# Kernel tuning notes

Measured on AMD Instinct MI355X. Metric: run time of the kernel, lower is better.

Reference implementation:

```python
import jax, jax.numpy as jnp
import numpy as np

DIM = 1024
N_STATE = 64
T, B = 512, 32


def _xavier(key, shape):
    fan_out, fan_in = shape
    limit = np.sqrt(6.0 / (fan_in + fan_out)).astype(np.float32)
    return jax.random.uniform(key, shape, jnp.float32, -limit, limit)


def setup_inputs() -> dict:
    key = jax.random.key(0)
    ks = jax.random.split(key, 5)
    return {
        "x": jax.random.normal(ks[0], (T, B, DIM), jnp.float32),
        "S": jnp.zeros((B, N_STATE, N_STATE), jnp.float32),
        "W_k": _xavier(ks[1], (N_STATE, DIM)),
        "W_v": _xavier(ks[2], (N_STATE, DIM)),
        "W_q": _xavier(ks[3], (N_STATE, DIM)),
        "W_alpha": _xavier(ks[4], (N_STATE, DIM)),
        "d_alpha": jnp.full((N_STATE,), 0.1, jnp.float32),
        "b_alpha": jnp.full((N_STATE,), 2.0, jnp.float32),
    }


def reference(x, S, W_k, W_v, W_q, W_alpha, d_alpha, b_alpha):
    # Precompute all projections as batched GEMMs: [T,B,n_state]
    k = jnp.einsum("tbd,nd->tbn", x, W_k)
    v = jnp.einsum("tbd,nd->tbn", x, W_v)
    q = jnp.einsum("tbd,nd->tbn", x, W_q)
    ax = jnp.einsum("tbd,nd->tbn", x, W_alpha)

    def step(S, inp):
        k_t, v_t, q_t, ax_t = inp  # each [B, n_state]
        retrieved = jnp.einsum("bij,bj->bi", S, k_t)          # S @ k
        alpha = jax.nn.sigmoid(ax_t + d_alpha * retrieved + b_alpha)
        # S = alpha * S + (1 - alpha) * outer(v, k); alpha gates rows
        S_new = alpha[:, :, None] * S + (1.0 - alpha)[:, :, None] * (
            v_t[:, :, None] * k_t[:, None, :]
        )
        h = jnp.einsum("bij,bj->bi", S_new, q_t)              # S @ q
        out_t = h * jax.nn.silu(h)                             # self-gated output
        return S_new, out_t

    S_final, output = jax.lax.scan(step, S, (k, v, q, ax))
    return output, S_final
```

## Files before the change

### kernel.cpp

```cpp
#include <hip/hip_runtime.h>
#include <hip/hip_bf16.h>

#define T_STEPS 512
#define BATCH 32
#define NST 64
#define DIM 1024

typedef _Float16 f16x8 __attribute__((ext_vector_type(8)));
typedef _Float16 f16x4 __attribute__((ext_vector_type(4)));
typedef float f32x4 __attribute__((ext_vector_type(4)));
typedef float f32x2 __attribute__((ext_vector_type(2)));

__device__ __forceinline__ void gl_lds16(const void* g, void* l) {
  __builtin_amdgcn_global_load_lds(
      (const __attribute__((address_space(1))) void*)g,
      (__attribute__((address_space(3))) void*)l, 16, 0, 0);
}

__global__ __launch_bounds__(256) void wconv(
    const float* __restrict__ Wk, const float* __restrict__ Wv,
    const float* __restrict__ Wq, const float* __restrict__ Wa,
    _Float16* __restrict__ Wc) {
  const int n = blockIdx.x;
  const int g = n >> 6, r = n & 63;
  const float* W = (g == 0) ? Wk : (g == 1) ? Wq : (g == 2) ? Wv : Wa;
  const float sc = (g == 3) ? -1.44269504088896340736f : 1.0f;
  float4 v = *(const float4*)(W + (size_t)r * DIM + threadIdx.x * 4);
  f16x4 h = {(_Float16)(v.x * sc), (_Float16)(v.y * sc), (_Float16)(v.z * sc),
             (_Float16)(v.w * sc)};
  *(f16x4*)(Wc + (size_t)n * DIM + threadIdx.x * 4) = h;
}

__global__ __launch_bounds__(512) void proj_gemm(
    const float* __restrict__ x, const _Float16* __restrict__ Wc,
    float* __restrict__ projf) {
  const int m0 = blockIdx.x * 64;
  const int tid = threadIdx.x;
  const int lane = tid & 63, wv = tid >> 6;
  const int wm = wv >> 2, wn = wv & 3;
  const int fm = lane & 15, fq = lane >> 4;

  __shared__ __align__(16) _Float16 Bl[2][256 * 32];
  __shared__ __align__(16) _Float16 Al[2][64 * 32];

  const int brow = tid >> 2;
  const int bcg = (tid & 3) ^ ((tid >> 3) & 3);
  const _Float16* gB = Wc + (size_t)brow * DIM + bcg * 8;
  const int bdst = tid * 8;

#define STAGE_B(buf, k0)                                          \
  {                                                               \
    _Pragma("unroll") for (int i = 0; i < 2; ++i)                 \
        gl_lds16(gB + (size_t)i * 128 * DIM + (k0),               \
                 &Bl[buf][i * 4096 + bdst]);                      \
  }

  const int arow = tid >> 3;
  const int afc = (tid & 7) * 4;
  const float* gA = x + (size_t)(m0 + arow) * DIM + afc;
  const int awp = arow * 32 + ((((tid >> 1) & 3) ^ ((arow >> 1) & 3)) * 8) +
                  (tid & 1) * 4;

#define LOADX(rr, k0)                          \
  {                                            \
    rr = *(const float4*)(gA + (k0));          \
  }
#define CVT_WRITE_A(buf, rr)                                        \
  {                                                                 \
    f16x4 h = {(_Float16)rr.x, (_Float16)rr.y, (_Float16)rr.z,      \
               (_Float16)rr.w};                                     \
    *(f16x4*)&Al[buf][awp] = h;                                     \
  }

  f32x4 acc[2][4];
#pragma unroll
  for (int mi = 0; mi < 2; ++mi)
#pragma unroll
    for (int ni = 0; ni < 4; ++ni) acc[mi][ni] = (f32x4){0.f, 0.f, 0.f, 0.f};

  const int aswz = (fq ^ ((fm >> 1) & 3)) * 8;
  const int abase = (wm * 32 + fm) * 32 + aswz;
  const int bbase = (wn * 64 + fm) * 32 + aswz;

#define COMPUTE(cb)                                                     \
  {                                                                     \
    f16x8 afr[2], bfr[4];                                               \
    _Pragma("unroll") for (int mi = 0; mi < 2; ++mi)                    \
        afr[mi] = *(const f16x8*)&Al[cb][abase + mi * 16 * 32];         \
    _Pragma("unroll") for (int ni = 0; ni < 4; ++ni)                    \
        bfr[ni] = *(const f16x8*)&Bl[cb][bbase + ni * 16 * 32];         \
    _Pragma("unroll") for (int mi = 0; mi < 2; ++mi)                    \
        _Pragma("unroll") for (int ni = 0; ni < 4; ++ni)                \
            acc[mi][ni] = __builtin_amdgcn_mfma_f32_16x16x32_f16(       \
                afr[mi], bfr[ni], acc[mi][ni], 0, 0, 0);                \
  }

  float4 rE, rO;
  LOADX(rE, 0);
  STAGE_B(0, 0);
  LOADX(rO, 32);
  CVT_WRITE_A(0, rE);
  __syncthreads();

  for (int k2 = 0; k2 < 16; ++k2) {
    STAGE_B(1, (2 * k2 + 1) * 32);
    if (k2 < 15) LOADX(rE, (2 * k2 + 2) * 32);
    CVT_WRITE_A(1, rO);
    COMPUTE(0);
    __syncthreads();
    if (k2 < 15) {
      STAGE_B(0, (2 * k2 + 2) * 32);
      LOADX(rO, (2 * k2 + 3) * 32);
      CVT_WRITE_A(0, rE);
    }
    COMPUTE(1);
    __syncthreads();
  }
#undef STAGE_B
#undef LOADX
#undef CVT_WRITE_A
#undef COMPUTE

#pragma unroll
  for (int mi = 0; mi < 2; ++mi)
#pragma unroll
    for (int ni = 0; ni < 4; ++ni) {
      const int gcol = wn * 64 + ni * 16 + fm;
      const int pcol = gcol < 128 ? gcol
                     : (gcol < 192 ? 128 + 2 * (gcol - 128) : 129 + 2 * (gcol - 192));
#pragma unroll
      for (int r = 0; r < 4; ++r) {
        const int grow = m0 + wm * 32 + mi * 16 + fq * 4 + r;
        projf[(size_t)grow * 256 + pcol] = acc[mi][ni][r];
      }
    }
}

__device__ __forceinline__ float red16(float x) {
  int v = __builtin_amdgcn_update_dpp(0, __float_as_int(x), 0xB1, 0xF, 0xF, true);
  x += __int_as_float(v);
  v = __builtin_amdgcn_update_dpp(0, __float_as_int(x), 0x4E, 0xF, 0xF, true);
  x += __int_as_float(v);
  v = __builtin_amdgcn_update_dpp(0, __float_as_int(x), 0x124, 0xF, 0xF, true);
  x += __int_as_float(v);
  v = __builtin_amdgcn_update_dpp(0, __float_as_int(x), 0x128, 0xF, 0xF, true);
  x += __int_as_float(v);
  return x;
}

__global__ __launch_bounds__(512, 1) void scan_kernel(
    const float* __restrict__ projf, const float* __restrict__ S0,
    const float* __restrict__ d_alpha, const float* __restrict__ b_alpha,
    float* __restrict__ out, float* __restrict__ Sout) {
  const int b = blockIdx.x >> 2;
  const int rg = blockIdx.x & 3;
  const int tid = threadIdx.x;
  const bool prod = tid < 256;
  const int ptid = tid & 255;
  const int c = ptid & 15;
  const int lr = ptid >> 4;
  const int r = rg * 16 + lr;
  const int j0 = c * 4;

  __shared__ __align__(16) float lbuf[4][2048];
  __shared__ __align__(16) float2 alcc[2][8][16];

  constexpr float NL2E = -1.44269504088896340736f;
  f32x2 s01, s23;
  {
    float4 v = *(const float4*)(S0 + ((size_t)b * NST + r) * NST + j0);
    s01 = (f32x2){v.x, v.y}; s23 = (f32x2){v.z, v.w};
  }
  const float da2 = d_alpha[r] * NL2E;
  const float ba2 = b_alpha[r] * NL2E;

  const int sstep = tid >> 6;
  const int soff = (tid & 63) * 4;
  const int lidx = sstep * 256 + soff;
  const float* gp = projf + (size_t)b * 256;
#define GADDR(ch) (gp + (size_t)((ch) * 8 + sstep) * (BATCH * 256) + soff)

  float4 rA;
  rA = *(const float4*)GADDR(0); *(float4*)&lbuf[0][lidx] = rA;
  rA = *(const float4*)GADDR(1); *(float4*)&lbuf[1][lidx] = rA;
  rA = *(const float4*)GADDR(2);
  __syncthreads();

  f32x2 k01[2], k23[2], q01[2], q23[2], vaf[2];
#define PREFP(tn)                                                        \
  {                                                                      \
    const int pp = (tn) & 1;                                             \
    const float* Pn = &lbuf[((tn) >> 3) & 3][((tn) & 7) * 256];          \
    float4 kk = *(const float4*)(Pn + j0);                               \
    k01[pp] = (f32x2){kk.x, kk.y}; k23[pp] = (f32x2){kk.z, kk.w};        \
    float2 vv = *(const float2*)(Pn + 128 + 2 * r);                      \
    vaf[pp] = (f32x2){vv.x, vv.y};                                       \
  }
#define PREFC(tn)                                                        \
  {                                                                      \
    const int pp = (tn) & 1;                                             \
    const float* Pn = &lbuf[((tn) >> 3) & 3][((tn) & 7) * 256];          \
    float4 kk = *(const float4*)(Pn + j0);                               \
    k01[pp] = (f32x2){kk.x, kk.y}; k23[pp] = (f32x2){kk.z, kk.w};        \
    float4 qq = *(const float4*)(Pn + 64 + j0);                          \
    q01[pp] = (f32x2){qq.x, qq.y}; q23[pp] = (f32x2){qq.z, qq.w};        \
  }

  if (prod) { PREFP(0); } else { PREFC(0); }

  for (int ch = 0; ch <= 64; ++ch) {
    if (prod) {
      if (ch < 64) {
#pragma unroll
        for (int si = 0; si < 8; ++si) {
          const int t = ch * 8 + si;
          const int p = si & 1;
          if (t + 1 < T_STEPS) PREFP(t + 1);

          f32x2 pa = s01 * k01[p] + s23 * k23[p];
          const float rr = red16(pa[0] + pa[1]);

          float z2 = fmaf(da2, rr, vaf[p][1] + ba2);
          z2 = __builtin_amdgcn_fmed3f(z2, -43.3f, 43.3f);
          const float e = __builtin_amdgcn_exp2f(z2);
          const float al = __builtin_amdgcn_rcpf(1.f + e);
          const float cc = (e * vaf[p][0]) * al;

          const f32x2 al2 = {al, al}, cc2 = {cc, cc};
          s01 = al2 * s01 + cc2 * k01[p];
          s23 = al2 * s23 + cc2 * k23[p];

          if (c == 0) alcc[ch & 1][si][lr] = make_float2(al, cc);
        }
      }
    } else {
      if (ch >= 1) {
        const int pch = ch - 1;
#pragma unroll
        for (int si = 0; si < 8; ++si) {
          const int t = pch * 8 + si;
          const int p = si & 1;
          if (t + 1 < T_STEPS) PREFC(t + 1);

          float2 ac = alcc[pch & 1][si][lr];
          const f32x2 al2 = {ac.x, ac.x}, cc2 = {ac.y, ac.y};
          s01 = al2 * s01 + cc2 * k01[p];
          s23 = al2 * s23 + cc2 * k23[p];

          f32x2 hh = s01 * q01[p] + s23 * q23[p];
          const float h = red16(hh[0] + hh[1]);
          if (c == 0) {
            const float sg =
                __builtin_amdgcn_rcpf(1.f + __builtin_amdgcn_exp2f(h * NL2E));
            out[((size_t)t * BATCH + b) * NST + r] = (h * h) * sg;
          }
        }
      }
    }
    __syncthreads();
    if (ch + 2 < 64) *(float4*)&lbuf[(ch + 2) & 3][lidx] = rA;
    if (ch + 3 < 64) rA = *(const float4*)GADDR(ch + 3);
    __syncthreads();
  }
#undef PREFP
#undef PREFC
#undef GADDR

  if (!prod) {
    float4 o = {s01[0], s01[1], s23[0], s23[1]};
    *(float4*)(Sout + ((size_t)b * NST + r) * NST + j0) = o;
  }
}

extern "C" void kernel_launch(void* const* d_in, const int* in_sizes, int n_in,
                              void* d_out, int out_size, void* d_ws, size_t ws_size,
                              hipStream_t stream) {
  const float* x  = (const float*)d_in[0];
  const float* S0 = (const float*)d_in[1];
  const float* Wk = (const float*)d_in[2];
  const float* Wv = (const float*)d_in[3];
  const float* Wq = (const float*)d_in[4];
  const float* Wa = (const float*)d_in[5];
  const float* da = (const float*)d_in[6];
  const float* ba = (const float*)d_in[7];

  float* out  = (float*)d_out;
  float* Sout = out + (size_t)T_STEPS * BATCH * NST;
  float* projf = (float*)d_ws;
  _Float16* Wc = (_Float16*)((char*)d_ws + (size_t)16384 * 256 * 4);

  wconv<<<256, 256, 0, stream>>>(Wk, Wv, Wq, Wa, Wc);
  proj_gemm<<<256, 512, 0, stream>>>(x, Wc, projf);
  scan_kernel<<<4 * BATCH, 512, 0, stream>>>(projf, S0, da, ba, out, Sout);
}
```

Before: 210.6 us.

## Replace LDS staging of projections with direct register double-buffered global loads

The scan kernel stops staging projection chunks through a 32KB shared buffer. Producer and consumer threads now load their own k/v/q slices for 8 timesteps straight from global memory into register arrays, double-buffered across two chunks. The alpha/c handoff buffer is transposed so consumers can read all 8 steps for their row at once. This removes the LDS round trip and some copy work, but raises register pressure and may expose global load latency on the serial scan path.

```diff
diff --git a/kernel.cpp b/kernel.cpp
--- a/kernel.cpp
+++ b/kernel.cpp
@@ -162,8 +162,7 @@
   const int r = rg * 16 + lr;
   const int j0 = c * 4;
 
-  __shared__ __align__(16) float lbuf[4][2048];
-  __shared__ __align__(16) float2 alcc[2][8][16];
+  __shared__ __align__(16) float2 alcc[2][16][8];
 
   constexpr float NL2E = -1.44269504088896340736f;
   f32x2 s01, s23;
@@ -174,102 +173,102 @@
   const float da2 = d_alpha[r] * NL2E;
   const float ba2 = b_alpha[r] * NL2E;
 
-  const int sstep = tid >> 6;
-  const int soff = (tid & 63) * 4;
-  const int lidx = sstep * 256 + soff;
-  const float* gp = projf + (size_t)b * 256;
-#define GADDR(ch) (gp + (size_t)((ch) * 8 + sstep) * (BATCH * 256) + soff)
-
-  float4 rA;
-  rA = *(const float4*)GADDR(0); *(float4*)&lbuf[0][lidx] = rA;
-  rA = *(const float4*)GADDR(1); *(float4*)&lbuf[1][lidx] = rA;
-  rA = *(const float4*)GADDR(2);
-  __syncthreads();
-
-  f32x2 k01[2], k23[2], q01[2], q23[2], vaf[2];
-#define PREFP(tn)                                                        \
-  {                                                                      \
-    const int pp = (tn) & 1;                                             \
-    const float* Pn = &lbuf[((tn) >> 3) & 3][((tn) & 7) * 256];          \
-    float4 kk = *(const float4*)(Pn + j0);                               \
-    k01[pp] = (f32x2){kk.x, kk.y}; k23[pp] = (f32x2){kk.z, kk.w};        \
-    float2 vv = *(const float2*)(Pn + 128 + 2 * r);                      \
-    vaf[pp] = (f32x2){vv.x, vv.y};                                       \
-  }
-#define PREFC(tn)                                                        \
-  {                                                                      \
-    const int pp = (tn) & 1;                                             \
-    const float* Pn = &lbuf[((tn) >> 3) & 3][((tn) & 7) * 256];          \
-    float4 kk = *(const float4*)(Pn + j0);                               \
-    k01[pp] = (f32x2){kk.x, kk.y}; k23[pp] = (f32x2){kk.z, kk.w};        \
-    float4 qq = *(const float4*)(Pn + 64 + j0);                          \
-    q01[pp] = (f32x2){qq.x, qq.y}; q23[pp] = (f32x2){qq.z, qq.w};        \
-  }
-
-  if (prod) { PREFP(0); } else { PREFC(0); }
-
-  for (int ch = 0; ch <= 64; ++ch) {
+  const float* gb = projf + (size_t)b * 256;
+
+#define P_LOAD(karr, varr, chn)                                         \
+  {                                                                     \
+    const float* pb = gb + (size_t)(chn) * 65536;                       \
+    _Pragma("unroll") for (int si = 0; si < 8; ++si) {                  \
+      karr[si] = *(const float4*)(pb + si * 8192 + j0);                 \
+      varr[si] = *(const float2*)(pb + si * 8192 + 128 + 2 * r);        \
+    }                                                                   \
+  }
+#define C_LOAD(karr, qarr, chn)                                         \
+  {                                                                     \
+    const float* pb = gb + (size_t)(chn) * 65536;                       \
+    _Pragma("unroll") for (int si = 0; si < 8; ++si) {                  \
+      karr[si] = *(const float4*)(pb + si * 8192 + j0);                 \
+      qarr[si] = *(const float4*)(pb + si * 8192 + 64 + j0);            \
+    }                                                                   \
+  }
+
+#define P_COMP(karr, varr, abuf)                                        \
+  {                                                                     \
+    _Pragma("unroll") for (int si = 0; si < 8; ++si) {                  \
+      const f32x2 k01 = {karr[si].x, karr[si].y};                       \
+      const f32x2 k23 = {karr[si].z, karr[si].w};                       \
+      f32x2 pa = s01 * k01 + s23 * k23;                                 \
+      const float rr = red16(pa[0] + pa[1]);                            \
+      float z2 = fmaf(da2, rr, varr[si].y + ba2);                       \
+      z2 = __builtin_amdgcn_fmed3f(z2, -43.3f, 43.3f);                  \
+      const float e = __builtin_amdgcn_exp2f(z2);                       \
+      const float al = __builtin_amdgcn_rcpf(1.f + e);                  \
+      const float ccv = (e * varr[si].x) * al;                          \
+      const f32x2 al2 = {al, al}, cc2 = {ccv, ccv};                     \
+      s01 = al2 * s01 + cc2 * k01;                                      \
+      s23 = al2 * s23 + cc2 * k23;                                      \
+      if (c == 0) alcc[abuf][lr][si] = make_float2(al, ccv);            \
+    }                                                                   \
+  }
+#define C_COMP(karr, qarr, abuf, chn)                                   \
+  {                                                                     \
+    float2 acv[8];                                                      \
+    _Pragma("unroll") for (int si = 0; si < 8; ++si)                    \
+        acv[si] = alcc[abuf][lr][si];                                   \
+    _Pragma("unroll") for (int si = 0; si < 8; ++si) {                  \
+      const f32x2 k01 = {karr[si].x, karr[si].y};                       \
+      const f32x2 k23 = {karr[si].z, karr[si].w};                       \
+      const f32x2 al2 = {acv[si].x, acv[si].x};                         \
+      const f32x2 cc2 = {acv[si].y, acv[si].y};                         \
+      s01 = al2 * s01 + cc2 * k01;                                      \
+      s23 = al2 * s23 + cc2 * k23;                                      \
+      const f32x2 q01 = {qarr[si].x, qarr[si].y};                       \
+      const f32x2 q23 = {qarr[si].z, qarr[si].w};                       \
+      f32x2 hh = s01 * q01 + s23 * q23;                                 \
+      const float h = red16(hh[0] + hh[1]);                             \
+      if (c == 0) {                                                     \
+        const float sg =                                                \
+            __builtin_amdgcn_rcpf(1.f + __builtin_amdgcn_exp2f(h * NL2E)); \
+        out[((size_t)((chn) * 8 + si) * BATCH + b) * NST + r] = (h * h) * sg; \
+      }                                                                 \
+    }                                                                   \
+  }
+
+  float4 kA[8], kB[8];
+  float2 vA[8], vB[8];
+  float4 qA[8], qB[8];
+
+  if (prod) {
+    P_LOAD(kA, vA, 0);
+  }
+
+  for (int c2 = 0; c2 < 32; ++c2) {
     if (prod) {
-      if (ch < 64) {
-#pragma unroll
-        for (int si = 0; si < 8; ++si) {
-          const int t = ch * 8 + si;
-          const int p = si & 1;
-          if (t + 1 < T_STEPS) PREFP(t + 1);
-
-          f32x2 pa = s01 * k01[p] + s23 * k23[p];
-          const float rr = red16(pa[0] + pa[1]);
-
-          float z2 = fmaf(da2, rr, vaf[p][1] + ba2);
-          z2 = __builtin_amdgcn_fmed3f(z2, -43.3f, 43.3f);
-          const float e = __builtin_amdgcn_exp2f(z2);
-          const float al = __builtin_amdgcn_rcpf(1.f + e);
-          const float cc = (e * vaf[p][0]) * al;
-
-          const f32x2 al2 = {al, al}, cc2 = {cc, cc};
-          s01 = al2 * s01 + cc2 * k01[p];
-          s23 = al2 * s23 + cc2 * k23[p];
-
-          if (c == 0) alcc[ch & 1][si][lr] = make_float2(al, cc);
-        }
-      }
+      P_LOAD(kB, vB, 2 * c2 + 1);
+      P_COMP(kA, vA, 0);
     } else {
-      if (ch >= 1) {
-        const int pch = ch - 1;
-#pragma unroll
-        for (int si = 0; si < 8; ++si) {
-          const int t = pch * 8 + si;
-          const int p = si & 1;
-          if (t + 1 < T_STEPS) PREFC(t + 1);
-
-          float2 ac = alcc[pch & 1][si][lr];
-          const f32x2 al2 = {ac.x, ac.x}, cc2 = {ac.y, ac.y};
-          s01 = al2 * s01 + cc2 * k01[p];
-          s23 = al2 * s23 + cc2 * k23[p];
-
-          f32x2 hh = s01 * q01[p] + s23 * q23[p];
-          const float h = red16(hh[0] + hh[1]);
-          if (c == 0) {
-            const float sg =
-                __builtin_amdgcn_rcpf(1.f + __builtin_amdgcn_exp2f(h * NL2E));
-            out[((size_t)t * BATCH + b) * NST + r] = (h * h) * sg;
-          }
-        }
-      }
-    }
-    __syncthreads();
-    if (ch + 2 < 64) *(float4*)&lbuf[(ch + 2) & 3][lidx] = rA;
-    if (ch + 3 < 64) rA = *(const float4*)GADDR(ch + 3);
-    __syncthreads();
-  }
-#undef PREFP
-#undef PREFC
-#undef GADDR
-
+      C_LOAD(kA, qA, 2 * c2);
+      if (c2 > 0) C_COMP(kB, qB, 1, 2 * c2 - 1);
+    }
+    __syncthreads();
+    if (prod) {
+      if (c2 < 31) P_LOAD(kA, vA, 2 * c2 + 2);
+      P_COMP(kB, vB, 1);
+    } else {
+      C_LOAD(kB, qB, 2 * c2 + 1);
+      C_COMP(kA, qA, 0, 2 * c2);
+    }
+    __syncthreads();
+  }
   if (!prod) {
+    C_COMP(kB, qB, 1, 63);
     float4 o = {s01[0], s01[1], s23[0], s23[1]};
     *(float4*)(Sout + ((size_t)b * NST + r) * NST + j0) = o;
   }
+#undef P_LOAD
+#undef C_LOAD
+#undef P_COMP
+#undef C_COMP
 }
 
 extern "C" void kernel_launch(void* const* d_in, const int* in_sizes, int n_in,
```

After: 237.7 us. +12.9%, slower.

## Break scan dependency chain using precomputed consecutive-key dot products

Applied to the files above, without the earlier changes.

Adds a small kernel that computes k_{t-1}·k_t for every batch and timestep and stages it in LDS. The producer wavefront then computes the retrieval S_t·k_t algebraically from the previous step's quantities (alpha, e, v and the Gram value) plus a reduction on the already-updated state for the next key. This takes the cross-lane reduction off the critical serial path between consecutive steps. It costs an extra kernel launch, a deeper four-slot prefetch buffer, and a different floating-point summation order in the recurrence.

```diff
diff --git a/kernel.cpp b/kernel.cpp
--- a/kernel.cpp
+++ b/kernel.cpp
@@ -136,6 +136,27 @@
     }
 }
 
+__global__ __launch_bounds__(256) void gram_kernel(
+    const float* __restrict__ projf, float* __restrict__ gmat) {
+  const int b = blockIdx.x >> 1;
+  const int t = (blockIdx.x & 1) * 256 + threadIdx.x;
+  float acc = 0.f;
+  if (t > 0) {
+    const float* ka = projf + ((size_t)(t - 1) * BATCH + b) * 256;
+    const float* kb = projf + ((size_t)t * BATCH + b) * 256;
+#pragma unroll
+    for (int j = 0; j < 64; j += 4) {
+      float4 va = *(const float4*)(ka + j);
+      float4 vb = *(const float4*)(kb + j);
+      acc = fmaf(va.x, vb.x, acc);
+      acc = fmaf(va.y, vb.y, acc);
+      acc = fmaf(va.z, vb.z, acc);
+      acc = fmaf(va.w, vb.w, acc);
+    }
+  }
+  gmat[(size_t)b * T_STEPS + t] = acc;
+}
+
 __device__ __forceinline__ float red16(float x) {
   int v = __builtin_amdgcn_update_dpp(0, __float_as_int(x), 0xB1, 0xF, 0xF, true);
   x += __int_as_float(v);
@@ -149,7 +170,8 @@
 }
 
 __global__ __launch_bounds__(512, 1) void scan_kernel(
-    const float* __restrict__ projf, const float* __restrict__ S0,
+    const float* __restrict__ projf, const float* __restrict__ gmat,
+    const float* __restrict__ S0,
     const float* __restrict__ d_alpha, const float* __restrict__ b_alpha,
     float* __restrict__ out, float* __restrict__ Sout) {
   const int b = blockIdx.x >> 2;
@@ -164,6 +186,7 @@
 
   __shared__ __align__(16) float lbuf[4][2048];
   __shared__ __align__(16) float2 alcc[2][8][16];
+  __shared__ __align__(8) float glds[T_STEPS];
 
   constexpr float NL2E = -1.44269504088896340736f;
   f32x2 s01, s23;
@@ -180,33 +203,48 @@
   const float* gp = projf + (size_t)b * 256;
 #define GADDR(ch) (gp + (size_t)((ch) * 8 + sstep) * (BATCH * 256) + soff)
 
+  glds[tid] = gmat[(size_t)b * T_STEPS + tid];
+
   float4 rA;
   rA = *(const float4*)GADDR(0); *(float4*)&lbuf[0][lidx] = rA;
   rA = *(const float4*)GADDR(1); *(float4*)&lbuf[1][lidx] = rA;
   rA = *(const float4*)GADDR(2);
   __syncthreads();
 
-  f32x2 k01[2], k23[2], q01[2], q23[2], vaf[2];
+  float4 kf[4];
+  float2 vaf[4];
+  float gv[4];
 #define PREFP(tn)                                                        \
   {                                                                      \
-    const int pp = (tn) & 1;                                             \
+    const int pp = (tn) & 3;                                             \
     const float* Pn = &lbuf[((tn) >> 3) & 3][((tn) & 7) * 256];          \
-    float4 kk = *(const float4*)(Pn + j0);                               \
-    k01[pp] = (f32x2){kk.x, kk.y}; k23[pp] = (f32x2){kk.z, kk.w};        \
-    float2 vv = *(const float2*)(Pn + 128 + 2 * r);                      \
-    vaf[pp] = (f32x2){vv.x, vv.y};                                       \
-  }
+    kf[pp] = *(const float4*)(Pn + j0);                                  \
+    vaf[pp] = *(const float2*)(Pn + 128 + 2 * r);                        \
+    gv[pp] = glds[(tn)];                                                 \
+  }
+  float4 kc4[2], qc4[2];
 #define PREFC(tn)                                                        \
   {                                                                      \
     const int pp = (tn) & 1;                                             \
     const float* Pn = &lbuf[((tn) >> 3) & 3][((tn) & 7) * 256];          \
-    float4 kk = *(const float4*)(Pn + j0);                               \
-    k01[pp] = (f32x2){kk.x, kk.y}; k23[pp] = (f32x2){kk.z, kk.w};        \
-    float4 qq = *(const float4*)(Pn + 64 + j0);                          \
-    q01[pp] = (f32x2){qq.x, qq.y}; q23[pp] = (f32x2){qq.z, qq.w};        \
-  }
-
-  if (prod) { PREFP(0); } else { PREFC(0); }
+    kc4[pp] = *(const float4*)(Pn + j0);                                 \
+    qc4[pp] = *(const float4*)(Pn + 64 + j0);                            \
+  }
+
+  float al = 1.f, e = 0.f, vp = 0.f, u = 0.f;
+  f32x2 cck01 = {0.f, 0.f}, cck23 = {0.f, 0.f};
+  f32x2 kc01, kc23;
+
+  if (prod) {
+    PREFP(0);
+    PREFP(1);
+    kc01 = (f32x2){kf[0].x, kf[0].y};
+    kc23 = (f32x2){kf[0].z, kf[0].w};
+    f32x2 pa = s01 * kc01 + s23 * kc23;
+    u = red16(pa[0] + pa[1]);
+  } else {
+    PREFC(0);
+  }
 
   for (int ch = 0; ch <= 64; ++ch) {
     if (prod) {
@@ -214,23 +252,35 @@
 #pragma unroll
         for (int si = 0; si < 8; ++si) {
           const int t = ch * 8 + si;
-          const int p = si & 1;
-          if (t + 1 < T_STEPS) PREFP(t + 1);
-
-          f32x2 pa = s01 * k01[p] + s23 * k23[p];
-          const float rr = red16(pa[0] + pa[1]);
-
-          float z2 = fmaf(da2, rr, vaf[p][1] + ba2);
+          const int p = si & 3;
+          const int pn = (si + 1) & 3;
+          if (t + 2 < T_STEPS) PREFP(t + 2);
+
+          const float vt = vaf[p].x, axv = vaf[p].y;
+
+          const float w = fmaf(e, vp * gv[p], u);
+          const float rr = al * w;
+          float z2 = fmaf(da2, rr, axv + ba2);
           z2 = __builtin_amdgcn_fmed3f(z2, -43.3f, 43.3f);
-          const float e = __builtin_amdgcn_exp2f(z2);
-          const float al = __builtin_amdgcn_rcpf(1.f + e);
-          const float cc = (e * vaf[p][0]) * al;
-
-          const f32x2 al2 = {al, al}, cc2 = {cc, cc};
-          s01 = al2 * s01 + cc2 * k01[p];
-          s23 = al2 * s23 + cc2 * k23[p];
-
-          if (c == 0) alcc[ch & 1][si][lr] = make_float2(al, cc);
+          const float eN = __builtin_amdgcn_exp2f(z2);
+          const float alN = __builtin_amdgcn_rcpf(1.f + eN);
+          const float ccN = (eN * vt) * alN;
+
+          const f32x2 al2 = {al, al};
+          s01 = al2 * s01 + cck01;
+          s23 = al2 * s23 + cck23;
+
+          const f32x2 kn01 = {kf[pn].x, kf[pn].y};
+          const f32x2 kn23 = {kf[pn].z, kf[pn].w};
+          f32x2 ua = s01 * kn01 + s23 * kn23;
+          const float uN = red16(ua[0] + ua[1]);
+
+          if (c == 0) alcc[ch & 1][si][lr] = make_float2(alN, ccN);
+
+          const f32x2 cc2 = {ccN, ccN};
+          cck01 = cc2 * kc01; cck23 = cc2 * kc23;
+          kc01 = kn01; kc23 = kn23;
+          al = alN; e = eN; vp = vt; u = uN;
         }
       }
     } else {
@@ -244,10 +294,14 @@
 
           float2 ac = alcc[pch & 1][si][lr];
           const f32x2 al2 = {ac.x, ac.x}, cc2 = {ac.y, ac.y};
-          s01 = al2 * s01 + cc2 * k01[p];
-          s23 = al2 * s23 + cc2 * k23[p];
-
-          f32x2 hh = s01 * q01[p] + s23 * q23[p];
+          const f32x2 k01 = {kc4[p].x, kc4[p].y};
+          const f32x2 k23 = {kc4[p].z, kc4[p].w};
+          s01 = al2 * s01 + cc2 * k01;
+          s23 = al2 * s23 + cc2 * k23;
+
+          const f32x2 q01 = {qc4[p].x, qc4[p].y};
+          const f32x2 q23 = {qc4[p].z, qc4[p].w};
+          f32x2 hh = s01 * q01 + s23 * q23;
           const float h = red16(hh[0] + hh[1]);
           if (c == 0) {
             const float sg =
@@ -288,8 +342,10 @@
   float* Sout = out + (size_t)T_STEPS * BATCH * NST;
   float* projf = (float*)d_ws;
   _Float16* Wc = (_Float16*)((char*)d_ws + (size_t)16384 * 256 * 4);
+  float* gmat = (float*)((char*)d_ws + (size_t)16384 * 256 * 4 + 512 * 1024);
 
   wconv<<<256, 256, 0, stream>>>(Wk, Wv, Wq, Wa, Wc);
   proj_gemm<<<256, 512, 0, stream>>>(x, Wc, projf);
-  scan_kernel<<<4 * BATCH, 512, 0, stream>>>(projf, S0, da, ba, out, Sout);
-}
+  gram_kernel<<<64, 256, 0, stream>>>(projf, gmat);
+  scan_kernel<<<4 * BATCH, 512, 0, stream>>>(projf, gmat, S0, da, ba, out, Sout);
+}
```

New measurement: 221.3 us. +5.1%, slower.
